# Performance work log

Measured on AMD Instinct MI355X. Metric: run time of the kernel, lower is better.

The kernel has to match this reference:

```python
import jax, jax.numpy as jnp
import numpy as np

NUM_HEADS = 12
EPS = 1e-5


def setup_inputs() -> dict:
    key = jax.random.key(0)
    k0, k1, k2 = jax.random.split(key, 3)
    B, C, D = 2, 768, 14  # batch, hidden_size, img_size//16
    x = jax.random.normal(k0, (B, C, D, D, D), dtype=jnp.float32)
    norm_w = jnp.ones((C,), dtype=jnp.float32)
    norm_b = jnp.zeros((C,), dtype=jnp.float32)
    qkv_w = jax.random.normal(k1, (3 * C, C), dtype=jnp.float32) * 0.02
    out_w = jax.random.normal(k2, (C, C), dtype=jnp.float32) * 0.02
    out_b = jnp.zeros((C,), dtype=jnp.float32)
    return {"x": x, "norm_w": norm_w, "norm_b": norm_b,
            "qkv_w": qkv_w, "out_w": out_w, "out_b": out_b}


def reference(x, norm_w, norm_b, qkv_w, out_w, out_b):
    B, C, D, H, W = x.shape
    nh = NUM_HEADS
    dh = C // nh
    scale = dh ** -0.5

    # b c d h w -> b (d h w) c
    t = jnp.transpose(x, (0, 2, 3, 4, 1)).reshape(B, D * H * W, C)
    N = t.shape[1]

    # LayerNorm over channel dim
    mu = jnp.mean(t, axis=-1, keepdims=True)
    var = jnp.mean(jnp.square(t - mu), axis=-1, keepdims=True)
    tn = (t - mu) / jnp.sqrt(var + EPS) * norm_w + norm_b

    # qkv projection (no bias), split as (3, heads, dim_head)
    qkv = tn @ qkv_w.T                       # [B, N, 3C]
    qkv = qkv.reshape(B, N, 3, nh, dh)
    qkv = jnp.transpose(qkv, (2, 0, 3, 1, 4))  # [3, B, nh, N, dh]
    q, k, v = qkv[0], qkv[1], qkv[2]

    att = jax.nn.softmax(jnp.einsum('blxn,blyn->blxy', q, k) * scale, axis=-1)
    out = jnp.einsum('blxy,blyn->blxn', att, v)  # [B, nh, N, dh]

    out = jnp.transpose(out, (0, 2, 1, 3)).reshape(B, N, C)
    out = out @ out_w.T + out_b

    out = out.reshape(B, D, H, W, C)
    out = jnp.transpose(out, (0, 4, 1, 2, 3))  # b d h w c -> b c d h w
    return out + x
```

## Files before the change

### kernel.cpp

```cpp
#include <hip/hip_runtime.h>

typedef unsigned short u16;
typedef unsigned int u32;

#define SPA 2744
#define CH  768
#define NH  12
#define DH  64
#define BB  2
#define TC  2304
#define MTOT (BB*SPA)
#define LNB 343
#define CVTB 2304

typedef __bf16 bf16x8_t __attribute__((ext_vector_type(8)));
typedef __bf16 bf16x4_t __attribute__((ext_vector_type(4)));
typedef short  s16x4    __attribute__((ext_vector_type(4)));
typedef float  f32x4_t  __attribute__((ext_vector_type(4)));

static __device__ __forceinline__ u16 f2bf(float f) {
    union { float f; u32 u; } v; v.f = f;
    u32 u = v.u;
    u += 0x7fffu + ((u >> 16) & 1u);
    return (u16)(u >> 16);
}

static __device__ __forceinline__ void gld16(const u16* g, u16* l) {
    __builtin_amdgcn_global_load_lds(
        (const __attribute__((address_space(1))) u32*)(size_t)g,
        (__attribute__((address_space(3))) u32*)(u32)(size_t)l, 16, 0, 0);
}

__global__ __launch_bounds__(256) void cvtln_kernel(const float* __restrict__ qkv_w,
                                                    u16* __restrict__ qkvw_bf, int n4a,
                                                    const float* __restrict__ out_w,
                                                    u16* __restrict__ outw_bf,
                                                    const float* __restrict__ x,
                                                    const float* __restrict__ w,
                                                    const float* __restrict__ bta,
                                                    u16* __restrict__ tn) {
    int tid = threadIdx.x;
    if (blockIdx.x >= LNB) {
        int i = (blockIdx.x - LNB) * 256 + tid;
        const float* src; u16* dst; int idx;
        if (i < n4a) { src = qkv_w; dst = qkvw_bf; idx = i; }
        else { src = out_w; dst = outw_bf; idx = i - n4a; }
        float4 f = ((const float4*)src)[idx];
        uint2 o;
        o.x = (u32)f2bf(f.x) | ((u32)f2bf(f.y) << 16);
        o.y = (u32)f2bf(f.z) | ((u32)f2bf(f.w) << 16);
        ((uint2*)dst)[idx] = o;
        return;
    }
    int bid = blockIdx.x;
    __shared__ f32x4_t redS[4][4];
    __shared__ f32x4_t redQ[4][4];
    __shared__ u16 T[64][22];
    int grp = tid & 3, chl = tid >> 2;
    int wvi = tid >> 6, lane = tid & 63;
    int tok0 = bid * 16 + grp * 4;
    int b = tok0 / SPA, n = tok0 - b * SPA;
    const float* base = x + (size_t)b * CH * SPA + n;

    f32x4_t s4 = {0.f, 0.f, 0.f, 0.f}, q4 = {0.f, 0.f, 0.f, 0.f};
    for (int c0 = 0; c0 < CH; c0 += 64) {
        float4 v = *(const float4*)(base + (size_t)(c0 + chl) * SPA);
        s4[0] += v.x; s4[1] += v.y; s4[2] += v.z; s4[3] += v.w;
        q4[0] += v.x * v.x; q4[1] += v.y * v.y; q4[2] += v.z * v.z; q4[3] += v.w * v.w;
    }
#pragma unroll
    for (int m = 4; m <= 32; m <<= 1)
#pragma unroll
        for (int e = 0; e < 4; e++) {
            s4[e] += __shfl_xor(s4[e], m);
            q4[e] += __shfl_xor(q4[e], m);
        }
    if (lane < 4) { redS[wvi][lane] = s4; redQ[wvi][lane] = q4; }
    __syncthreads();
    f32x4_t st = redS[0][grp], qt = redQ[0][grp];
#pragma unroll
    for (int wv2 = 1; wv2 < 4; wv2++) {
        f32x4_t a = redS[wv2][grp], c = redQ[wv2][grp];
#pragma unroll
        for (int e = 0; e < 4; e++) { st[e] += a[e]; qt[e] += c[e]; }
    }
    f32x4_t mean4, rstd4;
#pragma unroll
    for (int e = 0; e < 4; e++) {
        mean4[e] = st[e] * (1.0f / CH);
        rstd4[e] = rsqrtf(qt[e] * (1.0f / CH) - mean4[e] * mean4[e] + 1e-5f);
    }

    int tokl = tid >> 4, qq = tid & 15;
    int g2 = bid * 16 + tokl;
    for (int c0 = 0; c0 < CH; c0 += 64) {
        __syncthreads();
        {
            int cc = c0 + chl;
            float4 v = *(const float4*)(base + (size_t)cc * SPA);
            float ws = w[cc], bs = bta[cc];
            union { u16 h4[4]; uint2 u; } pk;
            pk.h4[0] = f2bf((v.x - mean4[0]) * rstd4[0] * ws + bs);
            pk.h4[1] = f2bf((v.y - mean4[1]) * rstd4[1] * ws + bs);
            pk.h4[2] = f2bf((v.z - mean4[2]) * rstd4[2] * ws + bs);
            pk.h4[3] = f2bf((v.w - mean4[3]) * rstd4[3] * ws + bs);
            *(uint2*)(&T[chl][grp * 4]) = pk.u;
        }
        __syncthreads();
        union { u16 h[4]; uint2 u; } pk;
#pragma unroll
        for (int e = 0; e < 4; e++) pk.h[e] = T[qq * 4 + e][tokl];
        *(uint2*)(tn + (size_t)g2 * CH + c0 + qq * 4) = pk.u;
    }
}

__global__ __launch_bounds__(256, 4) void gemm_qkv(const u16* __restrict__ A,
                                                   const u16* __restrict__ Bw,
                                                   u16* __restrict__ out0,
                                                   u16* __restrict__ out1,
                                                   u16* __restrict__ out2) {
    const int M = MTOT, K = CH;
    __shared__ __align__(16) u16 As[128 * 32];
    __shared__ __align__(16) u16 Bs[128 * 32];
    int tid = threadIdx.x;
    int m0 = blockIdx.y * 128;
    int n0 = blockIdx.x * 128;
    int wv = tid >> 6, lane = tid & 63;
    int wm = (wv >> 1) * 64, wn = (wv & 1) * 64;
    int quad = lane >> 4, l16 = lane & 15;

    f32x4_t zero = {0.f, 0.f, 0.f, 0.f};
    f32x4_t acc[4][4];
#pragma unroll
    for (int i = 0; i < 4; i++)
#pragma unroll
        for (int j = 0; j < 4; j++) acc[i][j] = zero;

    int rl = lane >> 2, pos = lane & 3;
    int sw = (l16 >> 1) & 3;
    for (int k0 = 0; k0 < K; k0 += 32) {
        __syncthreads();
#pragma unroll
        for (int p = 0; p < 2; p++) {
            int rbase = p * 64 + wv * 16;
            int row = rbase + rl;
            int gch = pos ^ ((row >> 1) & 3);
            int gm = m0 + row; if (gm >= M) gm = M - 1;
            gld16(A + (size_t)gm * K + k0 + gch * 8, As + rbase * 32);
            gld16(Bw + (size_t)(n0 + row) * K + k0 + gch * 8, Bs + rbase * 32);
        }
        __syncthreads();
        bf16x8_t af[4], bfr[4];
#pragma unroll
        for (int i = 0; i < 4; i++)
            af[i] = *(const bf16x8_t*)(As + (wm + i * 16 + l16) * 32 + ((quad ^ sw) * 8));
#pragma unroll
        for (int j = 0; j < 4; j++)
            bfr[j] = *(const bf16x8_t*)(Bs + (wn + j * 16 + l16) * 32 + ((quad ^ sw) * 8));
#pragma unroll
        for (int i = 0; i < 4; i++)
#pragma unroll
            for (int j = 0; j < 4; j++)
                acc[i][j] = __builtin_amdgcn_mfma_f32_16x16x32_bf16(af[i], bfr[j], acc[i][j], 0, 0, 0);
    }

    int which = n0 / CH;
    int rb = n0 - which * CH;
    u16* base = (which == 0) ? out0 : ((which == 1) ? out1 : out2);
    float qs = (which == 0) ? 0.18033688011112042f : 1.0f;
#pragma unroll
    for (int i = 0; i < 4; i++)
#pragma unroll
        for (int r = 0; r < 4; r++) {
            int gm = m0 + wm + i * 16 + quad * 4 + r;
            if (gm < M) {
                int b = gm / SPA, n = gm - b * SPA;
#pragma unroll
                for (int j = 0; j < 4; j++) {
                    int rem = rb + wn + j * 16 + l16;
                    int h = rem >> 6, d = rem & 63;
                    base[((size_t)(b * NH + h) * SPA + n) * DH + d] = f2bf(acc[i][j][r] * qs);
                }
            }
        }
}

__global__ __launch_bounds__(256, 4) void gemm_out(const u16* __restrict__ A,
                                                   const u16* __restrict__ Bw,
                                                   const float* __restrict__ xres,
                                                   const float* __restrict__ ob,
                                                   float* __restrict__ fout) {
    const int M = MTOT, K = CH;
    __shared__ __align__(16) u16 As[128 * 32];
    __shared__ __align__(16) u16 Bs[64 * 32];
    int tid = threadIdx.x;
    int m0 = blockIdx.y * 128;
    int n0 = blockIdx.x * 64;
    int wv = tid >> 6, lane = tid & 63;
    int wm = (wv >> 1) * 64, wn = (wv & 1) * 32;
    int quad = lane >> 4, l16 = lane & 15;

    f32x4_t zero = {0.f, 0.f, 0.f, 0.f};
    f32x4_t acc[4][2];
#pragma unroll
    for (int i = 0; i < 4; i++)
#pragma unroll
        for (int j = 0; j < 2; j++) acc[i][j] = zero;

    int rl = lane >> 2, pos = lane & 3;
    int sw = (l16 >> 1) & 3;
    for (int k0 = 0; k0 < K; k0 += 32) {
        __syncthreads();
#pragma unroll
        for (int p = 0; p < 2; p++) {
            int rbase = p * 64 + wv * 16;
            int row = rbase + rl;
            int gch = pos ^ ((row >> 1) & 3);
            int gm = m0 + row; if (gm >= M) gm = M - 1;
            gld16(A + (size_t)gm * K + k0 + gch * 8, As + rbase * 32);
        }
        {
            int row = wv * 16 + rl;
            int gch = pos ^ ((row >> 1) & 3);
            gld16(Bw + (size_t)(n0 + row) * K + k0 + gch * 8, Bs + (wv * 16) * 32);
        }
        __syncthreads();
        bf16x8_t af[4], bfr[2];
#pragma unroll
        for (int i = 0; i < 4; i++)
            af[i] = *(const bf16x8_t*)(As + (wm + i * 16 + l16) * 32 + ((quad ^ sw) * 8));
#pragma unroll
        for (int j = 0; j < 2; j++)
            bfr[j] = *(const bf16x8_t*)(Bs + (wn + j * 16 + l16) * 32 + ((quad ^ sw) * 8));
#pragma unroll
        for (int i = 0; i < 4; i++)
#pragma unroll
            for (int j = 0; j < 2; j++)
                acc[i][j] = __builtin_amdgcn_mfma_f32_16x16x32_bf16(af[i], bfr[j], acc[i][j], 0, 0, 0);
    }

#pragma unroll
    for (int i = 0; i < 4; i++) {
        int gm0 = m0 + wm + i * 16 + quad * 4;
        if (gm0 < M) {
            int b = gm0 / SPA;
            int n = gm0 - b * SPA;
#pragma unroll
            for (int j = 0; j < 2; j++) {
                int gn = n0 + wn + j * 16 + l16;
                size_t xo = ((size_t)(b * CH + gn)) * SPA + n;
                float4 xv = *(const float4*)(xres + xo);
                float bias = ob[gn];
                float4 rr;
                rr.x = xv.x + bias + acc[i][j][0];
                rr.y = xv.y + bias + acc[i][j][1];
                rr.z = xv.z + bias + acc[i][j][2];
                rr.w = xv.w + bias + acc[i][j][3];
                *(float4*)(fout + xo) = rr;
            }
        }
    }
}

__global__ __launch_bounds__(256) void vtrans_kernel(const u16* __restrict__ v,
                                                     u16* __restrict__ vt) {
    __shared__ __align__(16) u16 T[64 * 72];
    int bh = blockIdx.y;
    int n0 = blockIdx.x * 64;
    int tid = threadIdx.x;
#pragma unroll
    for (int h = 0; h < 2; h++) {
        int chunk = tid + h * 256;
        int r = chunk >> 3, cs = chunk & 7;
        int n = n0 + r;
        int4 val = make_int4(0, 0, 0, 0);
        if (n < SPA) val = *(const int4*)(v + ((size_t)bh * SPA + n) * DH + cs * 8);
        *(int4*)(T + r * 72 + cs * 8) = val;
    }
    __syncthreads();
#pragma unroll
    for (int h = 0; h < 2; h++) {
        int chunk = tid + h * 256;
        int d = chunk >> 3, cs = chunk & 7;
        int nb = n0 + cs * 8;
        if (nb < SPA) {
            union { u16 s[8]; int4 v4; } tmp;
#pragma unroll
            for (int e = 0; e < 8; e++) tmp.s[e] = T[(cs * 8 + e) * 72 + d];
            *(int4*)(vt + ((size_t)bh * DH + d) * SPA + nb) = tmp.v4;
        }
    }
}

__global__ __launch_bounds__(256, 4) void attn_kernel(const u16* __restrict__ q,
                                                      const u16* __restrict__ k,
                                                      const u16* __restrict__ vt,
                                                      u16* __restrict__ out) {
    __shared__ __align__(16) u16 Kbuf[2][64 * 64];
    __shared__ __align__(16) u16 Vbuf[2][64 * 76];
    int g = blockIdx.x;
    int xcd = g & 7, slot = g >> 3;
    int bh = xcd * 3 + slot % 3;
    int qg = slot / 3;
    int b = bh / NH, h = bh - b * NH;
    int tid = threadIdx.x;
    int wv = tid >> 6, lane = tid & 63;
    int quad = lane >> 4, l16 = lane & 15;
    int qhalf = wv & 1, khalf = wv >> 1;
    int koff = khalf * 32;
    int q0w = qg * 64 + qhalf * 32;

    const u16* qgp = q + (size_t)bh * SPA * DH;
    const u16* kg = k + (size_t)bh * SPA * DH;
    const u16* vg = vt + (size_t)bh * DH * SPA;

    bf16x8_t bq[2][2];
    int qglob[2];
#pragma unroll
    for (int qf = 0; qf < 2; qf++) {
        int qq = q0w + qf * 16 + l16;
        qglob[qf] = qq;
        int qld = (qq < SPA) ? qq : (SPA - 1);
#pragma unroll
        for (int ks = 0; ks < 2; ks++)
            bq[qf][ks] = *(const bf16x8_t*)(qgp + (size_t)qld * DH + ks * 32 + quad * 8);
    }

    f32x4_t zero = {0.f, 0.f, 0.f, 0.f};
    f32x4_t o[2][4];
#pragma unroll
    for (int qf = 0; qf < 2; qf++)
#pragma unroll
        for (int i = 0; i < 4; i++) o[qf][i] = zero;
    f32x4_t lacc[2];
    lacc[0] = zero; lacc[1] = zero;
    s16x4 ones;
    ones[0] = ones[1] = ones[2] = ones[3] = (short)0x3F80;

    int rl8 = lane >> 3, pos8 = lane & 7;
    int sw8 = l16 & 7;
    int vd = tid >> 2, vc = (tid & 3) * 16;

#pragma unroll
    for (int p = 0; p < 2; p++) {
        int rbase = p * 32 + wv * 8;
        int row = rbase + rl8;
        int gch = pos8 ^ (row & 7);
        gld16(kg + (size_t)row * DH + gch * 8, Kbuf[0] + rbase * 64);
    }
#pragma unroll
    for (int s2 = 0; s2 < 2; s2++)
        *(int4*)(Vbuf[0] + vd * 76 + vc + s2 * 8) =
            *(const int4*)(vg + (size_t)vd * SPA + vc + s2 * 8);

    for (int si = 0; si < 43; si++) {
        __syncthreads();
        int cur = si & 1, nxt = cur ^ 1;
        int kv0 = si * 64;
        bool hn = (si < 42);
        int4 vp0, vp1;
        if (hn) {
            int kb = kv0 + 64;
#pragma unroll
            for (int p = 0; p < 2; p++) {
                int rbase = p * 32 + wv * 8;
                int row = rbase + rl8;
                int gch = pos8 ^ (row & 7);
                int kr = kb + row; if (kr >= SPA) kr = SPA - 1;
                gld16(kg + (size_t)kr * DH + gch * 8, Kbuf[nxt] + rbase * 64);
            }
            int c0 = kb + vc;
            int a0 = c0;      if (a0 > SPA - 8) a0 = SPA - 8;
            int a1 = c0 + 8;  if (a1 > SPA - 8) a1 = SPA - 8;
            vp0 = *(const int4*)(vg + (size_t)vd * SPA + a0);
            vp1 = *(const int4*)(vg + (size_t)vd * SPA + a1);
        }

        s16x4 bp[2][2];
#pragma unroll
        for (int i = 0; i < 2; i++) {
            const u16* krow = Kbuf[cur] + (koff + i * 16 + l16) * 64;
            bf16x8_t ak0 = *(const bf16x8_t*)(krow + ((quad ^ sw8) * 8));
            bf16x8_t ak1 = *(const bf16x8_t*)(krow + (((4 + quad) ^ sw8) * 8));
            f32x4_t s0 = __builtin_amdgcn_mfma_f32_16x16x32_bf16(ak0, bq[0][0], zero, 0, 0, 0);
            s0 = __builtin_amdgcn_mfma_f32_16x16x32_bf16(ak1, bq[0][1], s0, 0, 0, 0);
            f32x4_t s1 = __builtin_amdgcn_mfma_f32_16x16x32_bf16(ak0, bq[1][0], zero, 0, 0, 0);
            s1 = __builtin_amdgcn_mfma_f32_16x16x32_bf16(ak1, bq[1][1], s1, 0, 0, 0);
            bf16x4_t p0, p1;
            if (si != 42) {
#pragma unroll
                for (int r = 0; r < 4; r++) {
                    p0[r] = (__bf16)__builtin_amdgcn_exp2f(s0[r]);
                    p1[r] = (__bf16)__builtin_amdgcn_exp2f(s1[r]);
                }
            } else {
#pragma unroll
                for (int r = 0; r < 4; r++) {
                    float e0 = __builtin_amdgcn_exp2f(s0[r]);
                    float e1 = __builtin_amdgcn_exp2f(s1[r]);
                    bool bad = (kv0 + koff + i * 16 + quad * 4 + r) >= SPA;
                    p0[r] = (__bf16)(bad ? 0.f : e0);
                    p1[r] = (__bf16)(bad ? 0.f : e1);
                }
            }
            union { bf16x4_t b; s16x4 s; } u0, u1;
            u0.b = p0; u1.b = p1;
            bp[0][i] = u0.s; bp[1][i] = u1.s;
        }

        if (hn) {
            *(int4*)(Vbuf[nxt] + vd * 76 + vc)     = vp0;
            *(int4*)(Vbuf[nxt] + vd * 76 + vc + 8) = vp1;
        }

#pragma unroll
        for (int c = 0; c < 2; c++) {
            lacc[0] = __builtin_amdgcn_mfma_f32_16x16x16bf16_1k(ones, bp[0][c], lacc[0], 0, 0, 0);
            lacc[1] = __builtin_amdgcn_mfma_f32_16x16x16bf16_1k(ones, bp[1][c], lacc[1], 0, 0, 0);
#pragma unroll
            for (int i = 0; i < 4; i++) {
                s16x4 av = *(const s16x4*)(Vbuf[cur] + (i * 16 + l16) * 76 + koff + c * 16 + quad * 4);
                o[0][i] = __builtin_amdgcn_mfma_f32_16x16x16bf16_1k(av, bp[0][c], o[0][i], 0, 0, 0);
                o[1][i] = __builtin_amdgcn_mfma_f32_16x16x16bf16_1k(av, bp[1][c], o[1][i], 0, 0, 0);
            }
        }
    }

    __syncthreads();
    float* lsh = (float*)Vbuf;
    if (wv >= 2) {
        int base = ((wv - 2) * 64 + lane) * 36;
#pragma unroll
        for (int qf = 0; qf < 2; qf++)
#pragma unroll
            for (int i = 0; i < 4; i++)
                *(f32x4_t*)(lsh + base + qf * 16 + i * 4) = o[qf][i];
        lsh[base + 32] = lacc[0][0];
        lsh[base + 33] = lacc[1][0];
    }
    __syncthreads();
    if (wv < 2) {
        int base = (wv * 64 + lane) * 36;
#pragma unroll
        for (int qf = 0; qf < 2; qf++)
#pragma unroll
            for (int i = 0; i < 4; i++) {
                f32x4_t t = *(const f32x4_t*)(lsh + base + qf * 16 + i * 4);
#pragma unroll
                for (int r = 0; r < 4; r++) o[qf][i][r] += t[r];
            }
        float lsum[2];
        lsum[0] = lacc[0][0] + lsh[base + 32];
        lsum[1] = lacc[1][0] + lsh[base + 33];
#pragma unroll
        for (int qf = 0; qf < 2; qf++) {
            int qq = qglob[qf];
            if (qq < SPA) {
                float inv = 1.0f / lsum[qf];
                u16* op = out + ((size_t)(b * SPA + qq)) * CH + h * DH;
#pragma unroll
                for (int i = 0; i < 4; i++) {
                    bf16x4_t ov;
#pragma unroll
                    for (int r = 0; r < 4; r++) ov[r] = (__bf16)(o[qf][i][r] * inv);
                    *(bf16x4_t*)(op + i * 16 + quad * 4) = ov;
                }
            }
        }
    }
}

extern "C" void kernel_launch(void* const* d_in, const int* in_sizes, int n_in,
                              void* d_out, int out_size, void* d_ws, size_t ws_size,
                              hipStream_t stream) {
    const float* x      = (const float*)d_in[0];
    const float* norm_w = (const float*)d_in[1];
    const float* norm_b = (const float*)d_in[2];
    const float* qkv_w  = (const float*)d_in[3];
    const float* out_w  = (const float*)d_in[4];
    const float* out_b  = (const float*)d_in[5];
    float* out = (float*)d_out;

    char* ws = (char*)d_ws;
    size_t off = 0;
    auto alloc = [&](size_t bytes) -> void* {
        void* p = ws + off;
        off += (bytes + 255) & ~(size_t)255;
        return p;
    };
    u16* tn      = (u16*)alloc((size_t)MTOT * CH * 2);
    u16* qkvw_bf = (u16*)alloc((size_t)TC * CH * 2);
    u16* outw_bf = (u16*)alloc((size_t)CH * CH * 2);
    u16* qb      = (u16*)alloc((size_t)BB * NH * SPA * DH * 2);
    u16* kb      = (u16*)alloc((size_t)BB * NH * SPA * DH * 2);
    u16* vb      = (u16*)alloc((size_t)BB * NH * SPA * DH * 2);
    u16* vtb     = (u16*)alloc((size_t)BB * NH * SPA * DH * 2);
    u16* ao      = (u16*)alloc((size_t)MTOT * CH * 2);

    int n4a = TC * CH / 4;
    cvtln_kernel<<<LNB + CVTB, 256, 0, stream>>>(
        qkv_w, qkvw_bf, n4a, out_w, outw_bf, x, norm_w, norm_b, tn);
    gemm_qkv<<<dim3(TC / 128, (MTOT + 127) / 128), 256, 0, stream>>>(
        tn, qkvw_bf, qb, kb, vb);
    vtrans_kernel<<<dim3((SPA + 63) / 64, BB * NH), 256, 0, stream>>>(vb, vtb);
    attn_kernel<<<1032, 256, 0, stream>>>(qb, kb, vtb, ao);
    gemm_out<<<dim3(CH / 64, (MTOT + 127) / 128), 256, 0, stream>>>(
        ao, outw_bf, x, out_b, out);
}
```

Before: 233.2 us.

## Give each attention wave a full key tile and drop cross-wave reduction

Each wave now owns 32 distinct queries and processes all 64 keys of every K/V tile, instead of splitting keys across wave pairs. A block therefore covers 128 queries, and the grid shrinks from 1032 to 528 blocks. This amortizes each staged K/V tile over twice as many queries and removes the shared-memory partial-sum reduction and its two barriers at the end. In exchange there are fewer blocks to spread across the CUs, a possibly worse tail, and more live registers per wave for the larger probability fragment array.

```diff
diff --git a/kernel.cpp b/kernel.cpp
--- a/kernel.cpp
+++ b/kernel.cpp
@@ -306,9 +306,7 @@
     int tid = threadIdx.x;
     int wv = tid >> 6, lane = tid & 63;
     int quad = lane >> 4, l16 = lane & 15;
-    int qhalf = wv & 1, khalf = wv >> 1;
-    int koff = khalf * 32;
-    int q0w = qg * 64 + qhalf * 32;
+    int q0w = qg * 128 + wv * 32;
 
     const u16* qgp = q + (size_t)bh * SPA * DH;
     const u16* kg = k + (size_t)bh * SPA * DH;
@@ -376,10 +374,10 @@
             vp1 = *(const int4*)(vg + (size_t)vd * SPA + a1);
         }
 
-        s16x4 bp[2][2];
-#pragma unroll
-        for (int i = 0; i < 2; i++) {
-            const u16* krow = Kbuf[cur] + (koff + i * 16 + l16) * 64;
+        s16x4 bp[2][4];
+#pragma unroll
+        for (int i = 0; i < 4; i++) {
+            const u16* krow = Kbuf[cur] + (i * 16 + l16) * 64;
             bf16x8_t ak0 = *(const bf16x8_t*)(krow + ((quad ^ sw8) * 8));
             bf16x8_t ak1 = *(const bf16x8_t*)(krow + (((4 + quad) ^ sw8) * 8));
             f32x4_t s0 = __builtin_amdgcn_mfma_f32_16x16x32_bf16(ak0, bq[0][0], zero, 0, 0, 0);
@@ -398,7 +396,7 @@
                 for (int r = 0; r < 4; r++) {
                     float e0 = __builtin_amdgcn_exp2f(s0[r]);
                     float e1 = __builtin_amdgcn_exp2f(s1[r]);
-                    bool bad = (kv0 + koff + i * 16 + quad * 4 + r) >= SPA;
+                    bool bad = (kv0 + i * 16 + quad * 4 + r) >= SPA;
                     p0[r] = (__bf16)(bad ? 0.f : e0);
                     p1[r] = (__bf16)(bad ? 0.f : e1);
                 }
@@ -414,57 +412,30 @@
         }
 
 #pragma unroll
-        for (int c = 0; c < 2; c++) {
+        for (int c = 0; c < 4; c++) {
             lacc[0] = __builtin_amdgcn_mfma_f32_16x16x16bf16_1k(ones, bp[0][c], lacc[0], 0, 0, 0);
             lacc[1] = __builtin_amdgcn_mfma_f32_16x16x16bf16_1k(ones, bp[1][c], lacc[1], 0, 0, 0);
 #pragma unroll
             for (int i = 0; i < 4; i++) {
-                s16x4 av = *(const s16x4*)(Vbuf[cur] + (i * 16 + l16) * 76 + koff + c * 16 + quad * 4);
+                s16x4 av = *(const s16x4*)(Vbuf[cur] + (i * 16 + l16) * 76 + c * 16 + quad * 4);
                 o[0][i] = __builtin_amdgcn_mfma_f32_16x16x16bf16_1k(av, bp[0][c], o[0][i], 0, 0, 0);
                 o[1][i] = __builtin_amdgcn_mfma_f32_16x16x16bf16_1k(av, bp[1][c], o[1][i], 0, 0, 0);
             }
         }
     }
 
-    __syncthreads();
-    float* lsh = (float*)Vbuf;
-    if (wv >= 2) {
-        int base = ((wv - 2) * 64 + lane) * 36;
-#pragma unroll
-        for (int qf = 0; qf < 2; qf++)
-#pragma unroll
-            for (int i = 0; i < 4; i++)
-                *(f32x4_t*)(lsh + base + qf * 16 + i * 4) = o[qf][i];
-        lsh[base + 32] = lacc[0][0];
-        lsh[base + 33] = lacc[1][0];
-    }
-    __syncthreads();
-    if (wv < 2) {
-        int base = (wv * 64 + lane) * 36;
-#pragma unroll
-        for (int qf = 0; qf < 2; qf++)
+#pragma unroll
+    for (int qf = 0; qf < 2; qf++) {
+        int qq = qglob[qf];
+        if (qq < SPA) {
+            float inv = 1.0f / lacc[qf][0];
+            u16* op = out + ((size_t)(b * SPA + qq)) * CH + h * DH;
 #pragma unroll
             for (int i = 0; i < 4; i++) {
-                f32x4_t t = *(const f32x4_t*)(lsh + base + qf * 16 + i * 4);
-#pragma unroll
-                for (int r = 0; r < 4; r++) o[qf][i][r] += t[r];
-            }
-        float lsum[2];
-        lsum[0] = lacc[0][0] + lsh[base + 32];
-        lsum[1] = lacc[1][0] + lsh[base + 33];
-#pragma unroll
-        for (int qf = 0; qf < 2; qf++) {
-            int qq = qglob[qf];
-            if (qq < SPA) {
-                float inv = 1.0f / lsum[qf];
-                u16* op = out + ((size_t)(b * SPA + qq)) * CH + h * DH;
-#pragma unroll
-                for (int i = 0; i < 4; i++) {
-                    bf16x4_t ov;
-#pragma unroll
-                    for (int r = 0; r < 4; r++) ov[r] = (__bf16)(o[qf][i][r] * inv);
-                    *(bf16x4_t*)(op + i * 16 + quad * 4) = ov;
-                }
+                bf16x4_t ov;
+#pragma unroll
+                for (int r = 0; r < 4; r++) ov[r] = (__bf16)(o[qf][i][r] * inv);
+                *(bf16x4_t*)(op + i * 16 + quad * 4) = ov;
             }
         }
     }
@@ -503,7 +474,7 @@
     gemm_qkv<<<dim3(TC / 128, (MTOT + 127) / 128), 256, 0, stream>>>(
         tn, qkvw_bf, qb, kb, vb);
     vtrans_kernel<<<dim3((SPA + 63) / 64, BB * NH), 256, 0, stream>>>(vb, vtb);
-    attn_kernel<<<1032, 256, 0, stream>>>(qb, kb, vtb, ao);
+    attn_kernel<<<528, 256, 0, stream>>>(qb, kb, vtb, ao);
     gemm_out<<<dim3(CH / 64, (MTOT + 127) / 128), 256, 0, stream>>>(
         ao, outw_bf, x, out_b, out);
 }
```

After: 237.2 us. About the same (+1.7%).
